# Kernel tuning notes

Hardware: AMD Instinct MI355X
Metric: run time of the kernel (lower is better)

The kernel has to match this reference:

```python
import jax, jax.numpy as jnp
import numpy as np


def setup_inputs() -> dict:
    key = jax.random.key(0)
    x = jax.random.normal(key, (32, 64, 128, 128), dtype=jnp.float32)
    return {"x": x}


def reference(x) -> jnp.ndarray:
    # Inverse wavelet transform: x is [4B, C, H, W] -> [B, C, 2H, 2W]
    B4, C, H, W = x.shape
    B = B4 // 4
    x1 = x[0 * B:1 * B] * 0.5
    x2 = x[1 * B:2 * B] * 0.5
    x3 = x[2 * B:3 * B] * 0.5
    x4 = x[3 * B:4 * B] * 0.5
    # Values by (row parity p, col parity q) of output pixel (2i+p, 2j+q)
    e00 = x1 - x2 - x3 + x4  # even row, even col
    e01 = x1 + x2 - x3 - x4  # even row, odd col
    e10 = x1 - x2 + x3 - x4  # odd row, even col
    e11 = x1 + x2 + x3 + x4  # odd row, odd col
    top = jnp.stack([e00, e01], axis=-1)     # [B, C, H, W, 2]
    bot = jnp.stack([e10, e11], axis=-1)     # [B, C, H, W, 2]
    h = jnp.stack([top, bot], axis=3)        # [B, C, H, 2, W, 2]
    return h.reshape(B, C, 2 * H, 2 * W)
```

## Files before the change

### kernel.cpp

```cpp
#include <hip/hip_runtime.h>


typedef float f2 __attribute__((ext_vector_type(2)));
typedef float f4 __attribute__((ext_vector_type(4)));

constexpr int H = 128, W = 128;
constexpr int HW = H * W;
constexpr int OUT_ROW = 2 * W;
constexpr int OUT_PLANE = 4 * HW;
constexpr int PAIRS = 4;

__global__ __launch_bounds__(256) void iwt_kernel(const float* __restrict__ x,
                                                  float* __restrict__ out,
                                                  int quarter)
{
    __shared__ f4 lds[4 * 64];

    const int t    = threadIdx.x;
    const int wq   = t >> 6;
    const int lane = t & 63;

    const int cb  = blockIdx.x >> 4;
    const int ipg = blockIdx.x & 15;

    const float* xq = x + wq * quarter + cb * HW + (lane << 2);

    const int ii_rel = wq >> 1;
    const int p      = wq & 1;
    const int u      = (ii_rel << 5) + (lane >> 1);
    const int sub    = (lane & 1) << 1;
    const float* lbase = reinterpret_cast<const float*>(lds) + u * 4 + sub;
    float* obase = out + cb * OUT_PLANE + wq * OUT_ROW + (lane << 2);

#pragma unroll
    for (int it = 0; it < PAIRS; ++it) {
        const int ip = ipg * PAIRS + it;
        const int i0 = ip << 1;

        f4 v = *reinterpret_cast<const f4*>(xq + i0 * W);

        __syncthreads();
        lds[(wq << 6) + lane] = v;
        __syncthreads();

        f2 v1 = *reinterpret_cast<const f2*>(lbase + 0 * 256);
        f2 v2 = *reinterpret_cast<const f2*>(lbase + 1 * 256);
        f2 v3 = *reinterpret_cast<const f2*>(lbase + 2 * 256);
        f2 v4 = *reinterpret_cast<const f2*>(lbase + 3 * 256);

        float a1 = v1[0] * 0.5f, a2 = v2[0] * 0.5f, a3 = v3[0] * 0.5f, a4 = v4[0] * 0.5f;
        float b1 = v1[1] * 0.5f, b2 = v2[1] * 0.5f, b3 = v3[1] * 0.5f, b4 = v4[1] * 0.5f;

        f4 o;
        if (p == 0) {
            o[0] = a1 - a2 - a3 + a4;
            o[1] = a1 + a2 - a3 - a4;
            o[2] = b1 - b2 - b3 + b4;
            o[3] = b1 + b2 - b3 - b4;
        } else {
            o[0] = a1 - a2 + a3 - a4;
            o[1] = a1 + a2 + a3 + a4;
            o[2] = b1 - b2 + b3 - b4;
            o[3] = b1 + b2 + b3 + b4;
        }

        __builtin_nontemporal_store(o, reinterpret_cast<f4*>(obase + (i0 << 1) * OUT_ROW));
    }
}

extern "C" void kernel_launch(void* const* d_in, const int* in_sizes, int n_in,
                              void* d_out, int out_size, void* d_ws, size_t ws_size,
                              hipStream_t stream) {
    const float* x = (const float*)d_in[0];
    float* out = (float*)d_out;

    const int quarter = in_sizes[0] / 4;
    const int n_cb    = quarter / HW;
    const int grid    = n_cb * (H / 2 / PAIRS);
    const int block   = 256;

    iwt_kernel<<<grid, block, 0, stream>>>(x, out, quarter);
}
```

Before: 234.4 us.

## Use single-wave blocks with async global-to-LDS loads and staged vmcnt waits

Each block becomes a single 64-thread wavefront that issues all sixteen 16-byte loads for its eight input rows up front, using global_load_lds so the data goes straight into LDS. It then waits on vmcnt in stages and processes each row pair as its data arrives. Each thread now writes both the even and odd output rows, and the __syncthreads barriers are gone. This is meant to raise memory-level parallelism and overlap loads with compute, at the cost of 16KB of LDS per block and much smaller blocks, which may limit occupancy.

```diff
diff --git a/kernel.cpp b/kernel.cpp
--- a/kernel.cpp
+++ b/kernel.cpp
@@ -8,63 +8,61 @@
 constexpr int HW = H * W;
 constexpr int OUT_ROW = 2 * W;
 constexpr int OUT_PLANE = 4 * HW;
-constexpr int PAIRS = 4;
 
-__global__ __launch_bounds__(256) void iwt_kernel(const float* __restrict__ x,
-                                                  float* __restrict__ out,
-                                                  int quarter)
+__global__ __launch_bounds__(64) void iwt_kernel(const float* __restrict__ x,
+                                                 float* __restrict__ out,
+                                                 int quarter)
 {
-    __shared__ f4 lds[4 * 64];
+    __shared__ float lds[16 * 256];
 
-    const int t    = threadIdx.x;
-    const int wq   = t >> 6;
-    const int lane = t & 63;
+    const int lane = threadIdx.x;
+    const int cb   = blockIdx.x >> 4;
+    const int r0   = (blockIdx.x & 15) << 3;
 
-    const int cb  = blockIdx.x >> 4;
-    const int ipg = blockIdx.x & 15;
-
-    const float* xq = x + wq * quarter + cb * HW + (lane << 2);
-
-    const int ii_rel = wq >> 1;
-    const int p      = wq & 1;
-    const int u      = (ii_rel << 5) + (lane >> 1);
-    const int sub    = (lane & 1) << 1;
-    const float* lbase = reinterpret_cast<const float*>(lds) + u * 4 + sub;
-    float* obase = out + cb * OUT_PLANE + wq * OUT_ROW + (lane << 2);
+    const float* xbase = x + cb * HW + r0 * W + (lane << 2);
 
 #pragma unroll
-    for (int it = 0; it < PAIRS; ++it) {
-        const int ip = ipg * PAIRS + it;
-        const int i0 = ip << 1;
+    for (int p = 0; p < 4; ++p) {
+#pragma unroll
+        for (int q = 0; q < 4; ++q) {
+            const float* src = xbase + q * quarter + (p * 2) * W;
+            __builtin_amdgcn_global_load_lds(
+                (const __attribute__((address_space(1))) void*)src,
+                (__attribute__((address_space(3))) void*)&lds[(p * 4 + q) * 256],
+                16, 0, 0);
+        }
+    }
 
-        f4 v = *reinterpret_cast<const f4*>(xq + i0 * W);
+    float* obase = out + cb * OUT_PLANE + (lane << 2);
 
-        __syncthreads();
-        lds[(wq << 6) + lane] = v;
-        __syncthreads();
+#pragma unroll
+    for (int p = 0; p < 4; ++p) {
+        if      (p == 0) asm volatile("s_waitcnt vmcnt(12)" ::: "memory");
+        else if (p == 1) asm volatile("s_waitcnt vmcnt(8)"  ::: "memory");
+        else if (p == 2) asm volatile("s_waitcnt vmcnt(4)"  ::: "memory");
+        else             asm volatile("s_waitcnt vmcnt(0)"  ::: "memory");
 
-        f2 v1 = *reinterpret_cast<const f2*>(lbase + 0 * 256);
-        f2 v2 = *reinterpret_cast<const f2*>(lbase + 1 * 256);
-        f2 v3 = *reinterpret_cast<const f2*>(lbase + 2 * 256);
-        f2 v4 = *reinterpret_cast<const f2*>(lbase + 3 * 256);
+        const float* lp = &lds[p * 1024];
 
-        float a1 = v1[0] * 0.5f, a2 = v2[0] * 0.5f, a3 = v3[0] * 0.5f, a4 = v4[0] * 0.5f;
-        float b1 = v1[1] * 0.5f, b2 = v2[1] * 0.5f, b3 = v3[1] * 0.5f, b4 = v4[1] * 0.5f;
+#pragma unroll
+        for (int ii = 0; ii < 2; ++ii) {
+            f2 v1 = *reinterpret_cast<const f2*>(lp + 0 * 256 + ii * 128 + (lane << 1));
+            f2 v2 = *reinterpret_cast<const f2*>(lp + 1 * 256 + ii * 128 + (lane << 1));
+            f2 v3 = *reinterpret_cast<const f2*>(lp + 2 * 256 + ii * 128 + (lane << 1));
+            f2 v4 = *reinterpret_cast<const f2*>(lp + 3 * 256 + ii * 128 + (lane << 1));
 
-        f4 o;
-        if (p == 0) {
-            o[0] = a1 - a2 - a3 + a4;
-            o[1] = a1 + a2 - a3 - a4;
-            o[2] = b1 - b2 - b3 + b4;
-            o[3] = b1 + b2 - b3 - b4;
-        } else {
-            o[0] = a1 - a2 + a3 - a4;
-            o[1] = a1 + a2 + a3 + a4;
-            o[2] = b1 - b2 + b3 - b4;
-            o[3] = b1 + b2 + b3 + b4;
+            float a1 = v1[0] * 0.5f, a2 = v2[0] * 0.5f, a3 = v3[0] * 0.5f, a4 = v4[0] * 0.5f;
+            float b1 = v1[1] * 0.5f, b2 = v2[1] * 0.5f, b3 = v3[1] * 0.5f, b4 = v4[1] * 0.5f;
+
+            f4 oe = { a1 - a2 - a3 + a4, a1 + a2 - a3 - a4,
+                      b1 - b2 - b3 + b4, b1 + b2 - b3 - b4 };
+            f4 oo = { a1 - a2 + a3 - a4, a1 + a2 + a3 + a4,
+                      b1 - b2 + b3 - b4, b1 + b2 + b3 + b4 };
+
+            const int orow = 2 * (r0 + 2 * p + ii);
+            __builtin_nontemporal_store(oe, reinterpret_cast<f4*>(obase + orow * OUT_ROW));
+            __builtin_nontemporal_store(oo, reinterpret_cast<f4*>(obase + (orow + 1) * OUT_ROW));
         }
-
-        __builtin_nontemporal_store(o, reinterpret_cast<f4*>(obase + (i0 << 1) * OUT_ROW));
     }
 }
 
@@ -76,8 +74,8 @@
 
     const int quarter = in_sizes[0] / 4;
     const int n_cb    = quarter / HW;
-    const int grid    = n_cb * (H / 2 / PAIRS);
-    const int block   = 256;
+    const int grid    = n_cb * (H / 8);
+    const int block   = 64;
 
     iwt_kernel<<<grid, block, 0, stream>>>(x, out, quarter);
 }
```

New measurement: 235.1 us. Within noise of the previous version (+0.3%).
